# Optimization experiments

Hardware: AMD Instinct MI355X
Metric: run time of the kernel (lower is better)

## Reference

```python
import jax, jax.numpy as jnp
import numpy as np

# wav2vec-large feature extractor conv spec: (kernel, stride), 512 channels each
LAYERS = [(10, 5), (8, 4), (4, 2), (4, 2), (4, 2)]
C = 512
BLUR = 0.05   # geomloss SamplesLoss default
N_ITER = 50   # fixed sinkhorn iterations (reference for eps-scaling loop)


def conv1d(x, w, stride):
    # x: [B, Cin, T], w: [Cout, Cin, K]
    return jax.lax.conv_general_dilated(
        x, w, window_strides=(stride,), padding='VALID',
        dimension_numbers=('NCH', 'OIH', 'NCH'))


def group_norm1(x, gamma, beta, eps=1e-5):
    # GroupNorm with 1 group over [C, T] per sample, per-channel affine
    mu = x.mean(axis=(1, 2), keepdims=True)
    var = x.var(axis=(1, 2), keepdims=True)
    return (x - mu) * jax.lax.rsqrt(var + eps) * gamma[None, :, None] + beta[None, :, None]


def features(wav, Ws, gs, bs):
    h = wav[:, None, :]  # [B,1,T]
    for (k, s), W, g, b in zip(LAYERS, Ws, gs, bs):
        h = jax.nn.relu(group_norm1(conv1d(h, W, s), g, b))
    return h  # [B, 512, T']


def sq_cost(a, b):
    # 0.5 * ||a_i - b_j||^2  (geomloss p=2 cost); a:[B,N,D], b:[B,M,D]
    aa = (a * a).sum(-1)
    bb = (b * b).sum(-1)
    ab = jnp.einsum('bnd,bmd->bnm', a, b)
    return 0.5 * jnp.maximum(aa[:, :, None] + bb[:, None, :] - 2.0 * ab, 0.0)


def ot_eps(Cm, eps):
    # entropic OT with uniform weights, log-domain sinkhorn; Cm: [B,N,M]
    B, N, M = Cm.shape
    loga = jnp.full((B, N), -jnp.log(N), dtype=Cm.dtype)
    logb = jnp.full((B, M), -jnp.log(M), dtype=Cm.dtype)
    f0 = jnp.zeros((B, N), Cm.dtype)
    g0 = jnp.zeros((B, M), Cm.dtype)

    def body(carry, _):
        f, g = carry
        g = -eps * jax.nn.logsumexp(loga[:, :, None] + (f[:, :, None] - Cm) / eps, axis=1)
        f = -eps * jax.nn.logsumexp(logb[:, None, :] + (g[:, None, :] - Cm) / eps, axis=2)
        return (f, g), None

    (f, g), _ = jax.lax.scan(body, (f0, g0), None, length=N_ITER)
    a = jnp.exp(loga)
    b = jnp.exp(logb)
    return (a * f).sum(-1) + (b * g).sum(-1)  # [B]


def sinkhorn_divergence(x, y):
    eps = BLUR ** 2
    return (ot_eps(sq_cost(x, y), eps)
            - 0.5 * ot_eps(sq_cost(x, x), eps)
            - 0.5 * ot_eps(sq_cost(y, y), eps))


def setup_inputs() -> dict:
    key = jax.random.key(0)
    ks = jax.random.split(key, 20)
    B, T = 16, 32000
    inp = {
        'y_hat': jax.random.normal(ks[0], (B, T), jnp.float32),
        'y': jax.random.normal(ks[1], (B, T), jnp.float32),
    }
    cin = 1
    for i, (k, s) in enumerate(LAYERS):
        inp[f'W{i}'] = jax.random.normal(ks[2 + i], (C, cin, k), jnp.float32) * 0.05
        inp[f'g{i}'] = jnp.ones((C,), jnp.float32)
        inp[f'b{i}'] = jnp.zeros((C,), jnp.float32)
        cin = C
    return inp


def reference(y_hat, y, W0, W1, W2, W3, W4, g0, g1, g2, g3, g4, b0, b1, b2, b3, b4):
    Ws = [W0, W1, W2, W3, W4]
    gs = [g0, g1, g2, g3, g4]
    bs = [b0, b1, b2, b3, b4]
    fx = features(y_hat, Ws, gs, bs)  # [B,512,T'] -> point cloud N=512, D=T'
    fy = features(y, Ws, gs, bs)
    return sinkhorn_divergence(fx, fy)  # [B]
```

## Files before the change

kernel.cpp:

```cpp
#include <hip/hip_runtime.h>

typedef unsigned int uint;
typedef unsigned short ushort;
using half8v  = __attribute__((ext_vector_type(8))) _Float16;
using half4v  = __attribute__((ext_vector_type(4))) _Float16;
using float4v = __attribute__((ext_vector_type(4))) float;

#define EPS_SINK 0.0025f
#define INV_EPS_SINK 400.0f
#define EPS_LOG512 0.015595811562598769f

static const size_t O_W1   = 0ull;
static const size_t O_W2   = 4194304ull;
static const size_t O_W3   = 6291456ull;
static const size_t O_W4   = 8388608ull;
static const size_t O_H0   = 20971520ull;
static const size_t O_H1   = 125829120ull;
static const size_t O_H2   = 20971520ull;
static const size_t O_H3   = 34045952ull;
static const size_t O_FEATX= 152010752ull;
static const size_t O_FEATY= 158498816ull;
static const size_t O_STATS= 164986880ull;
static const size_t O_CXY  = 0ull;
static const size_t O_CTXY = 8388608ull;
static const size_t O_CXX  = 16777216ull;
static const size_t O_CYY  = 25165824ull;
static const size_t O_AAX  = 33554432ull;
static const size_t O_AAY  = 33587200ull;
static const size_t O_F    = 33619968ull;
static const size_t O_G    = 33718272ull;

#define GLOAD_LDS16(gp, lp) __builtin_amdgcn_global_load_lds( \
    (const __attribute__((address_space(1))) void*)(gp),       \
    (__attribute__((address_space(3))) void*)(lp), 16, 0, 0)

__global__ __launch_bounds__(256) void prep_w(
    const float* __restrict__ W1, const float* __restrict__ W2,
    const float* __restrict__ W3, const float* __restrict__ W4,
    _Float16* __restrict__ w1, _Float16* __restrict__ w2,
    _Float16* __restrict__ w3, _Float16* __restrict__ w4)
{
    const int layer = blockIdx.y;
    const int e = blockIdx.x * 256 + threadIdx.x;
    float v[8];
    _Float16* dh;
    if (layer == 0) {
        const float4 a = *(const float4*)(W1 + (size_t)e * 8);
        const float4 c = *(const float4*)(W1 + (size_t)e * 8 + 4);
        v[0]=a.x; v[1]=a.y; v[2]=a.z; v[3]=a.w; v[4]=c.x; v[5]=c.y; v[6]=c.z; v[7]=c.w;
        dh = w1;
    } else {
        if (e >= 131072) return;
        const float* W = (layer == 1) ? W2 : (layer == 2) ? W3 : W4;
        dh = (layer == 1) ? w2 : (layer == 2) ? w3 : w4;
        const int oc = e >> 8, icp = e & 255;
        const float4 a = *(const float4*)(W + ((size_t)oc * 512 + icp * 2) * 4);
        const float4 c = *(const float4*)(W + ((size_t)oc * 512 + icp * 2 + 1) * 4);
        v[0]=a.x; v[1]=c.x; v[2]=a.y; v[3]=c.y; v[4]=a.z; v[5]=c.z; v[6]=a.w; v[7]=c.w;
    }
    half8v hi;
#pragma unroll
    for (int k = 0; k < 8; ++k) hi[k] = (_Float16)v[k];
    *(half8v*)(dh + (size_t)e * 8) = hi;
}

__global__ __launch_bounds__(256) void conv0_store(
    const float* __restrict__ wav, const float* __restrict__ W0,
    _Float16* __restrict__ h0, float* __restrict__ stats)
{
    __shared__ float LW[5120];
    __shared__ float red[2][256];
    const int tid = threadIdx.x;
    for (int e = tid; e < 5120; e += 256) LW[e] = W0[e];

    const int b = blockIdx.y;
    const int t = blockIdx.x * 256 + tid;
    const bool valid = (t < 6399);
    float xv[10];
#pragma unroll
    for (int d = 0; d < 10; ++d) xv[d] = 0.f;
    if (valid) {
        const float* wp = wav + (size_t)b * 32000 + (size_t)t * 5;
#pragma unroll
        for (int d = 0; d < 10; ++d) xv[d] = wp[d];
    }
    __syncthreads();

    float lsum = 0.f, lsq = 0.f;
    _Float16* hb = h0 + (size_t)b * 512 * 6400;
    for (int oc = 0; oc < 512; ++oc) {
        float a = 0.f;
#pragma unroll
        for (int d = 0; d < 10; ++d) a += LW[oc * 10 + d] * xv[d];
        if (valid) {
            hb[(size_t)oc * 6400 + t] = (_Float16)a;
            lsum += a; lsq += a * a;
        }
    }
    red[0][tid] = lsum; red[1][tid] = lsq;
    __syncthreads();
    for (int s2 = 128; s2 > 0; s2 >>= 1) {
        if (tid < s2) { red[0][tid] += red[0][tid + s2]; red[1][tid] += red[1][tid + s2]; }
        __syncthreads();
    }
    if (tid == 0) {
        atomicAdd(&stats[2 * b], red[0][0]);
        atomicAdd(&stats[2 * b + 1], red[1][0]);
    }
}

__global__ __launch_bounds__(256) void norm_h0(
    _Float16* __restrict__ h0, const float* __restrict__ stats,
    const float* __restrict__ gamma, const float* __restrict__ beta)
{
    const int row = blockIdx.y;
    const int b = row >> 9, oc = row & 511;
    const int t8 = (blockIdx.x * 256 + threadIdx.x) * 8;
    if (t8 >= 6400) return;
    const float invN = 1.f / (512.f * 6399.f);
    const float mu = stats[2 * b] * invN;
    const float var = stats[2 * b + 1] * invN - mu * mu;
    const float rs = rsqrtf(var + 1e-5f);
    const float sc = rs * gamma[oc];
    const float sh = beta[oc] - mu * sc;
    _Float16* p = h0 + (size_t)row * 6400 + t8;
    half8v v = *(half8v*)p;
#pragma unroll
    for (int k = 0; k < 8; ++k) {
        const float f = (t8 + k < 6399) ? fmaxf((float)v[k] * sc + sh, 0.f) : 0.f;
        v[k] = (_Float16)f;
    }
    *(half8v*)p = v;
}

__global__ __launch_bounds__(256, 4) void conv1_mfma(
    const _Float16* __restrict__ h0,
    const _Float16* __restrict__ w1,
    _Float16* __restrict__ oh, float* __restrict__ stats1)
{
    __shared__ _Float16 LW[2][2][4][128][8];
    __shared__ float red[2][256];

    const int tid  = threadIdx.x;
    const int lane = tid & 63, wv = tid >> 6;
    const int m    = lane & 15, quad = lane >> 4;
    const int wv2  = wv >> 1, wvt = wv & 1;

    const int raw = blockIdx.x;
    const int cid = (raw & 7) * 104 + (raw >> 3);
    const int b   = cid / 52;
    const int r2  = cid - b * 52;
    const int xt  = r2 >> 2, yt = r2 & 3;
    const int ocb = yt * 128;
    const int t0  = xt * 128;
    const int Lout = 1598;

    float4v acc[4][4];
#pragma unroll
    for (int i = 0; i < 4; ++i)
#pragma unroll
        for (int j = 0; j < 4; ++j) acc[i][j] = (float4v){0.f, 0.f, 0.f, 0.f};

    const _Float16* hb = h0 + (size_t)b * 512 * 6400;
    const int gbase = t0 * 4;
    const _Float16* px = hb + (size_t)quad * 6400 + gbase + (wvt * 64 + m) * 4;

    const _Float16* wsrc[4];
#pragma unroll
    for (int r = 0; r < 4; ++r) {
        const int e = wv * 4 + r;
        const int oh2 = e & 1, q = (e >> 1) & 3, k32l = e >> 3;
        wsrc[r] = w1 + ((size_t)(ocb + oh2 * 64 + lane) * 512 + (k32l * 4 + q)) * 8;
    }
    auto stageW = [&](int buf) {
#pragma unroll
        for (int r = 0; r < 4; ++r) {
            const int e = wv * 4 + r;
            const int oh2 = e & 1, q = (e >> 1) & 3, k32l = e >> 3;
            GLOAD_LDS16(wsrc[r], &LW[buf][k32l][q][oh2 * 64][0]);
            wsrc[r] += 64;
        }
    };

    stageW(0);
    __syncthreads();

    for (int it = 0; it < 64; ++it) {
        const int buf = it & 1;
        if (it < 63) stageW(buf ^ 1);
#pragma unroll
        for (int k32l = 0; k32l < 2; ++k32l) {
            half8v a4[4], bfv[4];
#pragma unroll
            for (int i = 0; i < 4; ++i)
                a4[i] = *(const half8v*)&LW[buf][k32l][quad][wv2 * 64 + i * 16 + m][0];
            const _Float16* pr = px + (size_t)k32l * 25600;
#pragma unroll
            for (int j = 0; j < 4; ++j)
                bfv[j] = *(const half8v*)(pr + j * 64);
#pragma unroll
            for (int i = 0; i < 4; ++i)
#pragma unroll
                for (int j = 0; j < 4; ++j)
                    acc[i][j] = __builtin_amdgcn_mfma_f32_16x16x32_f16(a4[i], bfv[j], acc[i][j], 0, 0, 0);
        }
        px += 51200;
        __syncthreads();
    }

    float lsum = 0.f, lsq = 0.f;
    uint* ohU = (uint*)oh;
#pragma unroll
    for (int i = 0; i < 4; ++i) {
        const int ocb2 = ocb + wv2 * 64 + i * 16 + quad * 4;
#pragma unroll
        for (int j = 0; j < 4; ++j) {
            const int t = t0 + wvt * 64 + j * 16 + m;
            if (t < Lout) {
#pragma unroll
                for (int pr = 0; pr < 2; ++pr) {
                    const float v0 = acc[i][j][pr * 2], v1 = acc[i][j][pr * 2 + 1];
                    union { uint u; _Float16 h[2]; } pk;
                    pk.h[0] = (_Float16)v0; pk.h[1] = (_Float16)v1;
                    const uint p = (uint)((ocb2 >> 1) + pr);
                    ohU[((size_t)(b * 256 + p)) * Lout + t] = pk.u;
                    lsum += v0 + v1; lsq += v0 * v0 + v1 * v1;
                }
            }
        }
    }
    red[0][tid] = lsum; red[1][tid] = lsq;
    __syncthreads();
    for (int s2 = 128; s2 > 0; s2 >>= 1) {
        if (tid < s2) { red[0][tid] += red[0][tid + s2]; red[1][tid] += red[1][tid + s2]; }
        __syncthreads();
    }
    if (tid == 0) {
        atomicAdd(&stats1[2 * b], red[0][0]);
        atomicAdd(&stats1[2 * b + 1], red[1][0]);
    }
}

template <bool PAIRED>
__global__ __launch_bounds__(256, 4) void conv_mfma(
    const _Float16* __restrict__ x,
    const _Float16* __restrict__ w,
    _Float16* __restrict__ oh, _Float16* __restrict__ ofeat,
    float* __restrict__ stats, int Lin, int Lout, int nx)
{
    __shared__ _Float16 LW[2][2][4][128][8];
    __shared__ float red[2][256];

    const int tid  = threadIdx.x;
    const int lane = tid & 63, wv = tid >> 6;
    const int m    = lane & 15, quad = lane >> 4;
    const int wv2  = wv >> 1, wvt = wv & 1;

    const int raw = blockIdx.x;
    const int chunk = (nx * 64) >> 3;
    const int cid = (raw & 7) * chunk + (raw >> 3);
    const int perb = nx * 4;
    const int b   = cid / perb;
    const int r2  = cid - b * perb;
    const int xt  = r2 >> 2, yt = r2 & 3;
    const int ocb = yt * 128;
    const int t0  = xt * 64;

    float4v acc[4][2];
#pragma unroll
    for (int i = 0; i < 4; ++i)
#pragma unroll
        for (int j = 0; j < 2; ++j) acc[i][j] = (float4v){0.f, 0.f, 0.f, 0.f};

    const size_t rstride = (size_t)Lin * 2;
    const _Float16* px = x + ((size_t)(b * 256) + quad) * rstride
                           + t0 * 4 + (wvt * 32 + m) * 4;

    const _Float16* wsrc[4];
#pragma unroll
    for (int r = 0; r < 4; ++r) {
        const int e = wv * 4 + r;
        const int oh2 = e & 1, q = (e >> 1) & 3, k32l = e >> 3;
        wsrc[r] = w + ((size_t)(ocb + oh2 * 64 + lane) * 256 + (k32l * 4 + q)) * 8;
    }
    auto stageW = [&](int buf) {
#pragma unroll
        for (int r = 0; r < 4; ++r) {
            const int e = wv * 4 + r;
            const int oh2 = e & 1, q = (e >> 1) & 3, k32l = e >> 3;
            GLOAD_LDS16(wsrc[r], &LW[buf][k32l][q][oh2 * 64][0]);
            wsrc[r] += 64;
        }
    };

    stageW(0);
    __syncthreads();

    for (int it = 0; it < 32; ++it) {
        const int buf = it & 1;
        if (it < 31) stageW(buf ^ 1);
#pragma unroll
        for (int k32l = 0; k32l < 2; ++k32l) {
            half8v a4[4], bfv[2];
#pragma unroll
            for (int i = 0; i < 4; ++i)
                a4[i] = *(const half8v*)&LW[buf][k32l][quad][wv2 * 64 + i * 16 + m][0];
            const _Float16* pr = px + (size_t)k32l * 4 * rstride;
#pragma unroll
            for (int j = 0; j < 2; ++j)
                bfv[j] = *(const half8v*)(pr + j * 64);
#pragma unroll
            for (int i = 0; i < 4; ++i)
#pragma unroll
                for (int j = 0; j < 2; ++j)
                    acc[i][j] = __builtin_amdgcn_mfma_f32_16x16x32_f16(a4[i], bfv[j], acc[i][j], 0, 0, 0);
        }
        px += 8 * rstride;
        __syncthreads();
    }

    float lsum = 0.f, lsq = 0.f;
    uint* ohU = (uint*)oh;
#pragma unroll
    for (int i = 0; i < 4; ++i) {
        const int ocb2 = ocb + wv2 * 64 + i * 16 + quad * 4;
#pragma unroll
        for (int j = 0; j < 2; ++j) {
            const int t = t0 + wvt * 32 + j * 16 + m;
            if (t < Lout) {
                if (PAIRED) {
#pragma unroll
                    for (int pr = 0; pr < 2; ++pr) {
                        const float v0 = acc[i][j][pr * 2], v1 = acc[i][j][pr * 2 + 1];
                        union { uint u; _Float16 h[2]; } pk;
                        pk.h[0] = (_Float16)v0; pk.h[1] = (_Float16)v1;
                        const uint p = (uint)((ocb2 >> 1) + pr);
                        ohU[((size_t)(b * 256 + p)) * Lout + t] = pk.u;
                        lsum += v0 + v1; lsq += v0 * v0 + v1 * v1;
                    }
                } else {
#pragma unroll
                    for (int r = 0; r < 4; ++r) {
                        const float v = acc[i][j][r];
                        ofeat[((size_t)(b * 512 + ocb2 + r)) * 224 + t] = (_Float16)v;
                        lsum += v; lsq += v * v;
                    }
                }
            }
        }
    }
    red[0][tid] = lsum; red[1][tid] = lsq;
    __syncthreads();
    for (int s2 = 128; s2 > 0; s2 >>= 1) {
        if (tid < s2) { red[0][tid] += red[0][tid + s2]; red[1][tid] += red[1][tid + s2]; }
        __syncthreads();
    }
    if (tid == 0) {
        atomicAdd(&stats[2 * b], red[0][0]);
        atomicAdd(&stats[2 * b + 1], red[1][0]);
    }
}

__global__ __launch_bounds__(256) void norm_pair(
    uint* __restrict__ h, const float* __restrict__ stats,
    const float* __restrict__ gamma, const float* __restrict__ beta,
    int L, float invN)
{
    const int row = blockIdx.y;
    const int b = row >> 8, p = row & 255;
    const int t = blockIdx.x * 256 + threadIdx.x;
    if (t >= L) return;
    const int c0 = 2 * p, c1 = 2 * p + 1;
    const float mu = stats[2 * b] * invN;
    const float var = stats[2 * b + 1] * invN - mu * mu;
    const float rs = rsqrtf(var + 1e-5f);
    const float sc0 = rs * gamma[c0], sh0 = beta[c0] - mu * sc0;
    const float sc1 = rs * gamma[c1], sh1 = beta[c1] - mu * sc1;
    const size_t idx = (size_t)row * L + t;
    union { uint u; _Float16 h2[2]; } pk;
    pk.u = h[idx];
    const float n0 = fmaxf((float)pk.h2[0] * sc0 + sh0, 0.f);
    const float n1 = fmaxf((float)pk.h2[1] * sc1 + sh1, 0.f);
    pk.h2[0] = (_Float16)n0; pk.h2[1] = (_Float16)n1;
    h[idx] = pk.u;
}

__global__ __launch_bounds__(256) void norm_feat(
    _Float16* __restrict__ h, const float* __restrict__ stats,
    const float* __restrict__ gamma, const float* __restrict__ beta)
{
    const int row = blockIdx.y;
    const int b = row >> 9, oc = row & 511;
    const int t = threadIdx.x;
    if (t >= 198) return;
    const float invN = 1.f / (512.f * 198.f);
    const float mu = stats[2 * b] * invN;
    const float var = stats[2 * b + 1] * invN - mu * mu;
    const float rs = rsqrtf(var + 1e-5f);
    const float sc = rs * gamma[oc];
    const float sh = beta[oc] - mu * sc;
    const size_t i = (size_t)row * 224 + t;
    const float v = (float)h[i] * sc + sh;
    h[i] = (_Float16)(v > 0.f ? v : 0.f);
}

__global__ __launch_bounds__(256) void aa_kernel(
    const _Float16* __restrict__ fX, const _Float16* __restrict__ fY,
    float* __restrict__ aaX, float* __restrict__ aaY)
{
    const int wave = threadIdx.x >> 6, lane = threadIdx.x & 63;
    const int R = blockIdx.x * 4 + wave;
    const _Float16* f = (R < 8192) ? fX : fY;
    const int r = R & 8191;
    const _Float16* row = f + (size_t)r * 224;
    float s = 0.f;
    if (lane < 56) {
        const half4v v = *(const half4v*)(row + lane * 4);
#pragma unroll
        for (int k = 0; k < 4; ++k) { const float x = (float)v[k]; s += x * x; }
    }
#pragma unroll
    for (int off = 32; off > 0; off >>= 1) s += __shfl_xor(s, off);
    if (lane == 0) ((R < 8192) ? aaX : aaY)[r] = s;
}

__global__ __launch_bounds__(256) void cost_kernel(
    const _Float16* __restrict__ fX, const _Float16* __restrict__ fY,
    const float* __restrict__ aaX, const float* __restrict__ aaY,
    _Float16* __restrict__ Cxy, _Float16* __restrict__ Cxx,
    _Float16* __restrict__ Cyy, _Float16* __restrict__ CTxy)
{
    const int z = blockIdx.y;
    const int mat = z >> 4, b = z & 15;
    const int nt = blockIdx.x & 3, mt = blockIdx.x >> 2;
    if (mat != 0 && nt > mt) return;
    const _Float16 *P, *Q; const float *aP, *aQ;
    _Float16 *Cm, *CT;
    if (mat == 0)      { P = fX; Q = fY; aP = aaX; aQ = aaY; Cm = Cxy; CT = CTxy; }
    else if (mat == 1) { P = fX; Q = fX; aP = aaX; aQ = aaX; Cm = Cxx; CT = (nt < mt) ? Cxx : nullptr; }
    else               { P = fY; Q = fY; aP = aaY; aQ = aaY; Cm = Cyy; CT = (nt < mt) ? Cyy : nullptr; }

    const int tid = threadIdx.x, lane = tid & 63, wv = tid >> 6;
    const int m16 = lane & 15, quad = lane >> 4;
    const int wv2 = wv >> 1, wvt = wv & 1;
    const int nb = nt * 128 + wv2 * 64;
    const int mb = mt * 128 + wvt * 64;
    const _Float16* Pb = P + (size_t)b * 512 * 224;
    const _Float16* Qb = Q + (size_t)b * 512 * 224;

    float4v acc[4][4];
#pragma unroll
    for (int i = 0; i < 4; ++i)
#pragma unroll
        for (int j = 0; j < 4; ++j) acc[i][j] = (float4v){0.f, 0.f, 0.f, 0.f};

    for (int k32 = 0; k32 < 7; ++k32) {
        const int ko = k32 * 32 + quad * 8;
        half8v a4[4], b4[4];
#pragma unroll
        for (int i = 0; i < 4; ++i)
            a4[i] = *(const half8v*)(Pb + (size_t)(nb + i * 16 + m16) * 224 + ko);
#pragma unroll
        for (int j = 0; j < 4; ++j)
            b4[j] = *(const half8v*)(Qb + (size_t)(mb + j * 16 + m16) * 224 + ko);
#pragma unroll
        for (int i = 0; i < 4; ++i)
#pragma unroll
            for (int j = 0; j < 4; ++j)
                acc[i][j] = __builtin_amdgcn_mfma_f32_16x16x32_f16(a4[i], b4[j], acc[i][j], 0, 0, 0);
    }

#pragma unroll
    for (int i = 0; i < 4; ++i) {
        const int nrow0 = nb + i * 16 + quad * 4;
        float aa4[4];
#pragma unroll
        for (int r = 0; r < 4; ++r) aa4[r] = aP[b * 512 + nrow0 + r];
#pragma unroll
        for (int j = 0; j < 4; ++j) {
            const int mcol = mb + j * 16 + m16;
            const float bbm = aQ[b * 512 + mcol];
#pragma unroll
            for (int r = 0; r < 4; ++r) {
                const int n = nrow0 + r;
                float c = 50.f * fmaxf(aa4[r] + bbm - 2.f * acc[i][j][r], 0.f);
                c = fminf(c, 65000.f);
                const _Float16 ch = (_Float16)c;
                Cm[((size_t)(b * 512 + n)) * 512 + mcol] = ch;
                if (CT) CT[((size_t)(b * 512 + mcol)) * 512 + n] = ch;
            }
        }
    }
}

static __device__ __forceinline__ void sink_rows(
    float* __restrict__ dst, const float* __restrict__ src,
    const _Float16* __restrict__ Mb, int p, int i0, int lane)
{
    const float* sp = src + (size_t)p * 512;
    float s8[8];
    {
        const float4 sa = *(const float4*)&sp[lane * 8];
        const float4 sb = *(const float4*)&sp[lane * 8 + 4];
        s8[0]=sa.x*400.f; s8[1]=sa.y*400.f; s8[2]=sa.z*400.f; s8[3]=sa.w*400.f;
        s8[4]=sb.x*400.f; s8[5]=sb.y*400.f; s8[6]=sb.z*400.f; s8[7]=sb.w*400.f;
    }
#pragma unroll
    for (int rr = 0; rr < 4; ++rr) {
        const int i = i0 + rr;
        const half8v rv = *(const half8v*)(Mb + (size_t)i * 512 + lane * 8);
        float a8[8];
#pragma unroll
        for (int k = 0; k < 8; ++k) a8[k] = fmaf(-4.f, (float)rv[k], s8[k]);
        float mx = a8[0];
#pragma unroll
        for (int k = 1; k < 8; ++k) mx = fmaxf(mx, a8[k]);
#pragma unroll
        for (int off = 32; off > 0; off >>= 1) mx = fmaxf(mx, __shfl_xor(mx, off));
        float ss = 0.f;
#pragma unroll
        for (int k = 0; k < 8; ++k) ss += __expf(a8[k] - mx);
#pragma unroll
        for (int off = 32; off > 0; off >>= 1) ss += __shfl_xor(ss, off);
        if (lane == 0)
            dst[(size_t)p * 512 + i] = EPS_LOG512 - EPS_SINK * (mx + logf(ss));
    }
}

__global__ __launch_bounds__(256) void sink_update(
    float* __restrict__ dst, const float* __restrict__ src,
    const _Float16* __restrict__ M0, const _Float16* __restrict__ M1,
    const _Float16* __restrict__ M2)
{
    const int p = blockIdx.y;
    const int mat = p >> 4, b = p & 15;
    const _Float16* M = ((mat == 0) ? M0 : ((mat == 1) ? M1 : M2)) + (size_t)b * 512 * 512;
    const int wave = threadIdx.x >> 6, lane = threadIdx.x & 63;
    const int i0 = blockIdx.x * 16 + wave * 4;
    sink_rows(dst, src, M, p, i0, lane);
}

__global__ __launch_bounds__(256) void final_kernel(
    const float* __restrict__ f, const float* __restrict__ g,
    float* __restrict__ out)
{
    const int b = blockIdx.x, tid = threadIdx.x;
    __shared__ float red[256];
    float a = 0.f;
    for (int n = tid; n < 512; n += 256) {
        const float xy = f[(0 * 16 + b) * 512 + n] + g[(0 * 16 + b) * 512 + n];
        const float xx = f[(1 * 16 + b) * 512 + n] + g[(1 * 16 + b) * 512 + n];
        const float yy = f[(2 * 16 + b) * 512 + n] + g[(2 * 16 + b) * 512 + n];
        a += xy - 0.5f * (xx + yy);
    }
    red[tid] = a;
    __syncthreads();
    for (int s2 = 128; s2 > 0; s2 >>= 1) {
        if (tid < s2) red[tid] += red[tid + s2];
        __syncthreads();
    }
    if (tid == 0) out[b] = red[0] * (1.0f / 512.0f);
}

extern "C" void kernel_launch(void* const* d_in, const int* in_sizes, int n_in,
                              void* d_out, int out_size, void* d_ws, size_t ws_size,
                              hipStream_t stream)
{
    (void)in_sizes; (void)n_in; (void)out_size; (void)ws_size;
    char* ws = (char*)d_ws;
    const float* yhat = (const float*)d_in[0];
    const float* ysig = (const float*)d_in[1];
    const float* Wl[5]; const float* gl[5]; const float* bl[5];
    for (int i = 0; i < 5; ++i) {
        Wl[i] = (const float*)d_in[2 + 3 * i];
        gl[i] = (const float*)d_in[3 + 3 * i];
        bl[i] = (const float*)d_in[4 + 3 * i];
    }
    float* out = (float*)d_out;
    float* statsA = (float*)(ws + O_STATS);

    _Float16* w1 = (_Float16*)(ws + O_W1);
    _Float16* w2 = (_Float16*)(ws + O_W2);
    _Float16* w3 = (_Float16*)(ws + O_W3);
    _Float16* w4 = (_Float16*)(ws + O_W4);
    _Float16* h0 = (_Float16*)(ws + O_H0);
    _Float16* h1 = (_Float16*)(ws + O_H1);
    _Float16* h2 = (_Float16*)(ws + O_H2);
    _Float16* h3 = (_Float16*)(ws + O_H3);

    hipMemsetAsync(statsA, 0, 512 * sizeof(float), stream);
    hipMemsetAsync(ws + O_FEATX, 0, 16 * 512 * 224 * 2, stream);
    hipMemsetAsync(ws + O_FEATY, 0, 16 * 512 * 224 * 2, stream);
    prep_w<<<dim3(1024, 4), 256, 0, stream>>>(Wl[1], Wl[2], Wl[3], Wl[4],
        w1, w2, w3, w4);

    for (int s = 0; s < 2; ++s) {
        const float* wav = (s == 0) ? yhat : ysig;
        float* st = statsA + (size_t)s * 160;
        _Float16* ft = (_Float16*)(ws + ((s == 0) ? O_FEATX : O_FEATY));

        conv0_store<<<dim3(25, 16), 256, 0, stream>>>(wav, Wl[0], h0, st);
        norm_h0<<<dim3(4, 8192), 256, 0, stream>>>(h0, st, gl[0], bl[0]);

        conv1_mfma<<<dim3(832), 256, 0, stream>>>(h0, w1, h1, st + 32);
        norm_pair<<<dim3(7, 4096), 256, 0, stream>>>(
            (uint*)h1, st + 32, gl[1], bl[1], 1598, 1.f / (512.f * 1598.f));

        conv_mfma<true><<<dim3(832), 256, 0, stream>>>(
            h1, w2, h2, nullptr, st + 64, 1598, 798, 13);
        norm_pair<<<dim3(4, 4096), 256, 0, stream>>>(
            (uint*)h2, st + 64, gl[2], bl[2], 798, 1.f / (512.f * 798.f));

        conv_mfma<true><<<dim3(448), 256, 0, stream>>>(
            h2, w3, h3, nullptr, st + 96, 798, 398, 7);
        norm_pair<<<dim3(2, 4096), 256, 0, stream>>>(
            (uint*)h3, st + 96, gl[3], bl[3], 398, 1.f / (512.f * 398.f));

        conv_mfma<false><<<dim3(256), 256, 0, stream>>>(
            h3, w4, nullptr, ft, st + 128, 398, 198, 4);
        norm_feat<<<dim3(1, 8192), 256, 0, stream>>>(
            ft, st + 128, gl[4], bl[4]);
    }

    _Float16* featX = (_Float16*)(ws + O_FEATX);
    _Float16* featY = (_Float16*)(ws + O_FEATY);
    aa_kernel<<<4096, 256, 0, stream>>>(featX, featY, (float*)(ws + O_AAX), (float*)(ws + O_AAY));
    cost_kernel<<<dim3(16, 48), 256, 0, stream>>>(
        featX, featY, (float*)(ws + O_AAX), (float*)(ws + O_AAY),
        (_Float16*)(ws + O_CXY), (_Float16*)(ws + O_CXX), (_Float16*)(ws + O_CYY),
        (_Float16*)(ws + O_CTXY));

    hipMemsetAsync(ws + O_F, 0, 2 * 24576 * sizeof(float), stream);

    float* fptr = (float*)(ws + O_F);
    float* gptr = (float*)(ws + O_G);
    _Float16* cxy  = (_Float16*)(ws + O_CXY);
    _Float16* ctxy = (_Float16*)(ws + O_CTXY);
    _Float16* cxx  = (_Float16*)(ws + O_CXX);
    _Float16* cyy  = (_Float16*)(ws + O_CYY);

    for (int it = 0; it < 50; ++it) {
        sink_update<<<dim3(32, 48), 256, 0, stream>>>(gptr, fptr, ctxy, cxx, cyy);
        sink_update<<<dim3(32, 48), 256, 0, stream>>>(fptr, gptr, cxy, cxx, cyy);
    }

    final_kernel<<<16, 256, 0, stream>>>(fptr, gptr, out);
}
```

Measured before the change: 1.847 ms.

## Fuse GroupNorm+ReLU into consumer conv operand loads and double-buffer activation loads

Removes the standalone norm_h0 and norm_pair kernels. Each consumer conv kernel now builds per-channel scale and shift in shared memory from the producer's statistics, then applies the affine transform and ReLU in fp16 to the activation vectors just before the MFMAs. This saves a full read-modify-write pass over each large intermediate activation, plus several launches per signal. conv_mfma also gets a register double-buffer for activation loads alongside the LDS weight ping-pong. The trade-off is extra fp16 ALU work inside the MFMA loop, the normalization now running in fp16 rather than fp32, and padded tail elements no longer being zeroed explicitly.

```diff
diff --git a/kernel.cpp b/kernel.cpp
--- a/kernel.cpp
+++ b/kernel.cpp
@@ -109,36 +109,15 @@
     }
 }
 
-__global__ __launch_bounds__(256) void norm_h0(
-    _Float16* __restrict__ h0, const float* __restrict__ stats,
-    const float* __restrict__ gamma, const float* __restrict__ beta)
-{
-    const int row = blockIdx.y;
-    const int b = row >> 9, oc = row & 511;
-    const int t8 = (blockIdx.x * 256 + threadIdx.x) * 8;
-    if (t8 >= 6400) return;
-    const float invN = 1.f / (512.f * 6399.f);
-    const float mu = stats[2 * b] * invN;
-    const float var = stats[2 * b + 1] * invN - mu * mu;
-    const float rs = rsqrtf(var + 1e-5f);
-    const float sc = rs * gamma[oc];
-    const float sh = beta[oc] - mu * sc;
-    _Float16* p = h0 + (size_t)row * 6400 + t8;
-    half8v v = *(half8v*)p;
-#pragma unroll
-    for (int k = 0; k < 8; ++k) {
-        const float f = (t8 + k < 6399) ? fmaxf((float)v[k] * sc + sh, 0.f) : 0.f;
-        v[k] = (_Float16)f;
-    }
-    *(half8v*)p = v;
-}
-
 __global__ __launch_bounds__(256, 4) void conv1_mfma(
     const _Float16* __restrict__ h0,
     const _Float16* __restrict__ w1,
+    const float* __restrict__ stats0,
+    const float* __restrict__ gamma0, const float* __restrict__ beta0,
     _Float16* __restrict__ oh, float* __restrict__ stats1)
 {
     __shared__ _Float16 LW[2][2][4][128][8];
+    __shared__ float LSC[512], LSH[512];
     __shared__ float red[2][256];
 
     const int tid  = threadIdx.x;
@@ -155,6 +134,18 @@
     const int t0  = xt * 128;
     const int Lout = 1598;
 
+    {
+        const float invN = 1.f / (512.f * 6399.f);
+        const float mu = stats0[2 * b] * invN;
+        const float var = stats0[2 * b + 1] * invN - mu * mu;
+        const float rs = rsqrtf(var + 1e-5f);
+        for (int ic = tid; ic < 512; ic += 256) {
+            const float sc = rs * gamma0[ic];
+            LSC[ic] = sc;
+            LSH[ic] = beta0[ic] - mu * sc;
+        }
+    }
+
     float4v acc[4][4];
 #pragma unroll
     for (int i = 0; i < 4; ++i)
@@ -194,10 +185,20 @@
 #pragma unroll
             for (int i = 0; i < 4; ++i)
                 a4[i] = *(const half8v*)&LW[buf][k32l][quad][wv2 * 64 + i * 16 + m][0];
+            const int ic = quad + 4 * k32l + 8 * it;
+            const _Float16 sch = (_Float16)LSC[ic];
+            const _Float16 shh = (_Float16)LSH[ic];
             const _Float16* pr = px + (size_t)k32l * 25600;
 #pragma unroll
-            for (int j = 0; j < 4; ++j)
-                bfv[j] = *(const half8v*)(pr + j * 64);
+            for (int j = 0; j < 4; ++j) {
+                half8v xv = *(const half8v*)(pr + j * 64);
+#pragma unroll
+                for (int k = 0; k < 8; ++k) {
+                    const _Float16 v = xv[k] * sch + shh;
+                    xv[k] = (v > (_Float16)0.f) ? v : (_Float16)0.f;
+                }
+                bfv[j] = xv;
+            }
 #pragma unroll
             for (int i = 0; i < 4; ++i)
 #pragma unroll
@@ -245,10 +246,13 @@
 __global__ __launch_bounds__(256, 4) void conv_mfma(
     const _Float16* __restrict__ x,
     const _Float16* __restrict__ w,
+    const float* __restrict__ statsP,
+    const float* __restrict__ gammaP, const float* __restrict__ betaP,
     _Float16* __restrict__ oh, _Float16* __restrict__ ofeat,
-    float* __restrict__ stats, int Lin, int Lout, int nx)
+    float* __restrict__ statsO, int Lin, int Lout, int nx)
 {
     __shared__ _Float16 LW[2][2][4][128][8];
+    __shared__ float LN[256][4];
     __shared__ float red[2][256];
 
     const int tid  = threadIdx.x;
@@ -266,6 +270,17 @@
     const int ocb = yt * 128;
     const int t0  = xt * 64;
 
+    {
+        const float invN = 1.f / (512.f * (float)Lin);
+        const float mu = statsP[2 * b] * invN;
+        const float var = statsP[2 * b + 1] * invN - mu * mu;
+        const float rs = rsqrtf(var + 1e-5f);
+        const int c0 = 2 * tid, c1 = 2 * tid + 1;
+        const float sc0 = rs * gammaP[c0], sc1 = rs * gammaP[c1];
+        LN[tid][0] = sc0; LN[tid][1] = betaP[c0] - mu * sc0;
+        LN[tid][2] = sc1; LN[tid][3] = betaP[c1] - mu * sc1;
+    }
+
     float4v acc[4][2];
 #pragma unroll
     for (int i = 0; i < 4; ++i)
@@ -292,30 +307,58 @@
             wsrc[r] += 64;
         }
     };
-
+    auto loadX = [&](half8v (&xr)[4], const _Float16* p) {
+#pragma unroll
+        for (int k32l = 0; k32l < 2; ++k32l)
+#pragma unroll
+            for (int j = 0; j < 2; ++j)
+                xr[k32l * 2 + j] = *(const half8v*)(p + (size_t)k32l * 4 * rstride + j * 64);
+    };
+    auto compute = [&](int buf, half8v (&xr)[4], int plB) {
+#pragma unroll
+        for (int k32l = 0; k32l < 2; ++k32l) {
+            half8v a4[4];
+#pragma unroll
+            for (int i = 0; i < 4; ++i)
+                a4[i] = *(const half8v*)&LW[buf][k32l][quad][wv2 * 64 + i * 16 + m][0];
+            const int pl = plB + quad + 4 * k32l;
+            const _Float16 s0 = (_Float16)LN[pl][0], h0v = (_Float16)LN[pl][1];
+            const _Float16 s1 = (_Float16)LN[pl][2], h1v = (_Float16)LN[pl][3];
+            half8v xn[2];
+#pragma unroll
+            for (int j = 0; j < 2; ++j) {
+                half8v xv = xr[k32l * 2 + j];
+#pragma unroll
+                for (int k = 0; k < 8; ++k) {
+                    const _Float16 v = xv[k] * ((k & 1) ? s1 : s0) + ((k & 1) ? h1v : h0v);
+                    xv[k] = (v > (_Float16)0.f) ? v : (_Float16)0.f;
+                }
+                xn[j] = xv;
+            }
+#pragma unroll
+            for (int i = 0; i < 4; ++i)
+#pragma unroll
+                for (int j = 0; j < 2; ++j)
+                    acc[i][j] = __builtin_amdgcn_mfma_f32_16x16x32_f16(a4[i], xn[j], acc[i][j], 0, 0, 0);
+        }
+    };
+
+    half8v xrA[4], xrB[4];
+    loadX(xrA, px); px += 8 * rstride;
     stageW(0);
     __syncthreads();
 
-    for (int it = 0; it < 32; ++it) {
-        const int buf = it & 1;
-        if (it < 31) stageW(buf ^ 1);
-#pragma unroll
-        for (int k32l = 0; k32l < 2; ++k32l) {
-            half8v a4[4], bfv[2];
-#pragma unroll
-            for (int i = 0; i < 4; ++i)
-                a4[i] = *(const half8v*)&LW[buf][k32l][quad][wv2 * 64 + i * 16 + m][0];
-            const _Float16* pr = px + (size_t)k32l * 4 * rstride;
-#pragma unroll
-            for (int j = 0; j < 2; ++j)
-                bfv[j] = *(const half8v*)(pr + j * 64);
-#pragma unroll
-            for (int i = 0; i < 4; ++i)
-#pragma unroll
-                for (int j = 0; j < 2; ++j)
-                    acc[i][j] = __builtin_amdgcn_mfma_f32_16x16x32_f16(a4[i], bfv[j], acc[i][j], 0, 0, 0);
+    for (int it = 0; it < 32; it += 2) {
+        stageW(1);
+        loadX(xrB, px); px += 8 * rstride;
+        compute(0, xrA, 8 * it);
+        __syncthreads();
+        if (it + 2 < 32) {
+            stageW(0);
+            loadX(xrA, px);
         }
         px += 8 * rstride;
+        compute(1, xrB, 8 * (it + 1));
         __syncthreads();
     }
 
@@ -356,33 +399,9 @@
         __syncthreads();
     }
     if (tid == 0) {
-        atomicAdd(&stats[2 * b], red[0][0]);
-        atomicAdd(&stats[2 * b + 1], red[1][0]);
-    }
-}
-
-__global__ __launch_bounds__(256) void norm_pair(
-    uint* __restrict__ h, const float* __restrict__ stats,
-    const float* __restrict__ gamma, const float* __restrict__ beta,
-    int L, float invN)
-{
-    const int row = blockIdx.y;
-    const int b = row >> 8, p = row & 255;
-    const int t = blockIdx.x * 256 + threadIdx.x;
-    if (t >= L) return;
-    const int c0 = 2 * p, c1 = 2 * p + 1;
-    const float mu = stats[2 * b] * invN;
-    const float var = stats[2 * b + 1] * invN - mu * mu;
-    const float rs = rsqrtf(var + 1e-5f);
-    const float sc0 = rs * gamma[c0], sh0 = beta[c0] - mu * sc0;
-    const float sc1 = rs * gamma[c1], sh1 = beta[c1] - mu * sc1;
-    const size_t idx = (size_t)row * L + t;
-    union { uint u; _Float16 h2[2]; } pk;
-    pk.u = h[idx];
-    const float n0 = fmaxf((float)pk.h2[0] * sc0 + sh0, 0.f);
-    const float n1 = fmaxf((float)pk.h2[1] * sc1 + sh1, 0.f);
-    pk.h2[0] = (_Float16)n0; pk.h2[1] = (_Float16)n1;
-    h[idx] = pk.u;
+        atomicAdd(&statsO[2 * b], red[0][0]);
+        atomicAdd(&statsO[2 * b + 1], red[1][0]);
+    }
 }
 
 __global__ __launch_bounds__(256) void norm_feat(
@@ -600,24 +619,19 @@
         _Float16* ft = (_Float16*)(ws + ((s == 0) ? O_FEATX : O_FEATY));
 
         conv0_store<<<dim3(25, 16), 256, 0, stream>>>(wav, Wl[0], h0, st);
-        norm_h0<<<dim3(4, 8192), 256, 0, stream>>>(h0, st, gl[0], bl[0]);
-
-        conv1_mfma<<<dim3(832), 256, 0, stream>>>(h0, w1, h1, st + 32);
-        norm_pair<<<dim3(7, 4096), 256, 0, stream>>>(
-            (uint*)h1, st + 32, gl[1], bl[1], 1598, 1.f / (512.f * 1598.f));
+
+        conv1_mfma<<<dim3(832), 256, 0, stream>>>(
+            h0, w1, st, gl[0], bl[0], h1, st + 32);
 
         conv_mfma<true><<<dim3(832), 256, 0, stream>>>(
-            h1, w2, h2, nullptr, st + 64, 1598, 798, 13);
-        norm_pair<<<dim3(4, 4096), 256, 0, stream>>>(
-            (uint*)h2, st + 64, gl[2], bl[2], 798, 1.f / (512.f * 798.f));
+            h1, w2, st + 32, gl[1], bl[1], h2, nullptr, st + 64, 1598, 798, 13);
 
         conv_mfma<true><<<dim3(448), 256, 0, stream>>>(
-            h2, w3, h3, nullptr, st + 96, 798, 398, 7);
-        norm_pair<<<dim3(2, 4096), 256, 0, stream>>>(
-            (uint*)h3, st + 96, gl[3], bl[3], 398, 1.f / (512.f * 398.f));
+            h2, w3, st + 64, gl[2], bl[2], h3, nullptr, st + 96, 798, 398, 7);
 
         conv_mfma<false><<<dim3(256), 256, 0, stream>>>(
-            h3, w4, nullptr, ft, st + 128, 398, 198, 4);
+            h3, w4, st + 96, gl[3], bl[3], nullptr, ft, st + 128, 398, 198, 4);
+
         norm_feat<<<dim3(1, 8192), 256, 0, stream>>>(
             ft, st + 128, gl[4], bl[4]);
     }
```

Result: faster. 1.691 ms (-8.5%).
